# Kernel optimization log

Hardware: AMD Instinct MI355X
Metric: run time of the kernel (lower is better)

## Reference

```python
import jax, jax.numpy as jnp
import numpy as np

B, N, D, H = 2, 64, 256, 8
DK = D // H
EPS = 1e-5


def layer_norm(x, g, b):
    mu = jnp.mean(x, axis=-1, keepdims=True)
    var = jnp.var(x, axis=-1, keepdims=True)
    return (x - mu) * jax.lax.rsqrt(var + EPS) * g + b


def setup_inputs() -> dict:
    key = jax.random.key(0)
    ks = jax.random.split(key, 12)
    s = 1.0 / np.sqrt(D)
    inp = {
        "x": jax.random.normal(ks[0], (B, N, N, D), jnp.float32),
        "W_lk": jax.random.uniform(ks[1], (D, D), jnp.float32, -s, s),
        "W_rk": jax.random.uniform(ks[2], (D, D), jnp.float32, -s, s),
        "W_lv": jax.random.uniform(ks[3], (D, D), jnp.float32, -s, s),
        "W_rv": jax.random.uniform(ks[4], (D, D), jnp.float32, -s, s),
        "W_out": jax.random.uniform(ks[5], (D, D), jnp.float32, -s, s),
        "ln_agg_g": jnp.ones((D,), jnp.float32),
        "ln_agg_b": jnp.zeros((D,), jnp.float32),
        "W1": jax.random.uniform(ks[6], (D, 2 * D), jnp.float32, -s, s),
        "b1": jnp.zeros((2 * D,), jnp.float32),
        "W2": jax.random.uniform(ks[7], (2 * D, D), jnp.float32, -1.0 / np.sqrt(2 * D), 1.0 / np.sqrt(2 * D)),
        "b2": jnp.zeros((D,), jnp.float32),
        "ln2_g": jnp.ones((D,), jnp.float32),
        "ln2_b": jnp.zeros((D,), jnp.float32),
    }
    return inp


def reference(x, W_lk, W_rk, W_lv, W_rv, W_out, ln_agg_g, ln_agg_b, W1, b1, W2, b2, ln2_g, ln2_b):
    b, n = x.shape[0], x.shape[1]
    # projections (no bias), split into heads: [b, n, n, H, DK]
    lk = (x @ W_lk).reshape(b, n, n, H, DK)
    rk = (x @ W_rk).reshape(b, n, n, H, DK)
    lv = (x @ W_lv).reshape(b, n, n, H, DK)
    rv = (x @ W_rv).reshape(b, n, n, H, DK)
    # triangle attention scores over intermediate node 'a'
    scores = jnp.einsum('bxahd,bayhd->bxayh', lk, rk) / np.sqrt(DK)
    att = jax.nn.softmax(scores, axis=2)
    # fused triangle value aggregation: sum_a att * lv[x,a] * rv[a,y]
    o = jnp.einsum('bxayh,bxahd,bayhd->bxyhd', att, lv, rv)
    o = o.reshape(b, n, n, D) @ W_out
    # FFN block (dropout = 0)
    h = layer_norm(x + o, ln_agg_g, ln_agg_b)
    m = jax.nn.relu(h @ W1 + b1) @ W2 + b2
    return layer_norm(m + h, ln2_g, ln2_b)
```

## Files before the change

### kernel.cpp

```cpp
#include <hip/hip_runtime.h>

#define ROWS 8192
#define DIM  256

typedef short short8 __attribute__((ext_vector_type(8)));
typedef float f4     __attribute__((ext_vector_type(4)));

__device__ __forceinline__ float bf2f(unsigned int u16) {
    union { unsigned int i; float f; } v;
    v.i = (u16 & 0xffffu) << 16;
    return v.f;
}
__device__ __forceinline__ unsigned short f2bf(float f) {
    union { float f; unsigned int u; } v; v.f = f;
    unsigned int r = v.u + 0x7fffu + ((v.u >> 16) & 1u);
    return (unsigned short)(r >> 16);
}

__global__ __launch_bounds__(256)
void cast_all(const float* __restrict__ x, unsigned short* __restrict__ xb,
              const float* __restrict__ w0, const float* __restrict__ w1,
              const float* __restrict__ w2, const float* __restrict__ w3,
              const float* __restrict__ w4, const float* __restrict__ w5,
              const float* __restrict__ w6, unsigned short* __restrict__ wt)
{
    if (blockIdx.x < 2048) {
        const size_t i = ((size_t)blockIdx.x * 256 + threadIdx.x) * 4;
        float4 v = *(const float4*)(x + i);
        uint2 p;
        p.x = f2bf(v.x) | ((unsigned int)f2bf(v.y) << 16);
        p.y = f2bf(v.z) | ((unsigned int)f2bf(v.w) << 16);
        *(uint2*)(xb + i) = p;
        return;
    }
    __shared__ float t[32][33];
    int id = blockIdx.x - 2048;
    const float* src; int K, N, Ntiles; size_t doff;
    if (id < 320) {
        int w = id >> 6; id &= 63; K = 256; N = 256; Ntiles = 8;
        doff = (size_t)w * 65536;
        src = (w == 0) ? w0 : (w == 1) ? w1 : (w == 2) ? w2 : (w == 3) ? w3 : w4;
    } else if (id < 448) {
        id -= 320; K = 256; N = 512; Ntiles = 16; doff = 327680; src = w5;
    } else {
        id -= 448; K = 512; N = 256; Ntiles = 8;  doff = 458752; src = w6;
    }
    const int tk = id / Ntiles, tn = id % Ntiles;
    const int k0 = tk * 32, n0 = tn * 32;
    const int c = threadIdx.x & 31, r8 = threadIdx.x >> 5;
    for (int rr = r8; rr < 32; rr += 8)
        t[rr][c] = src[(size_t)(k0 + rr) * N + n0 + c];
    __syncthreads();
    for (int rr = r8; rr < 32; rr += 8)
        wt[doff + (size_t)(n0 + rr) * K + k0 + c] = f2bf(t[c][rr]);
}

__global__ __launch_bounds__(256)
void proj_mfma(const unsigned short* __restrict__ A, const unsigned short* __restrict__ WT,
               unsigned short* __restrict__ projT)
{
    const int lane = threadIdx.x & 63, wave = threadIdx.x >> 6;
    const int wsel = blockIdx.x >> 2;
    const int col0 = (blockIdx.x & 3) * 64;
    const int m0 = blockIdx.y * 128 + wave * 32;
    const int lm = lane & 15, lk8 = (lane >> 4) * 8;
    const unsigned short* W = WT + (size_t)wsel * 65536;
    unsigned short* dst = projT + (size_t)wsel * 2097152;

    f4 acc[2][4];
    #pragma unroll
    for (int i = 0; i < 2; ++i)
        #pragma unroll
        for (int j = 0; j < 4; ++j) acc[i][j] = (f4){0.f, 0.f, 0.f, 0.f};

    #pragma unroll 2
    for (int kc = 0; kc < 256; kc += 32) {
        short8 af[2], bf[4];
        #pragma unroll
        for (int i = 0; i < 2; ++i)
            af[i] = *(const short8*)(A + (size_t)(m0 + i * 16 + lm) * 256 + kc + lk8);
        #pragma unroll
        for (int j = 0; j < 4; ++j)
            bf[j] = *(const short8*)(W + (size_t)(col0 + j * 16 + lm) * 256 + kc + lk8);
        #pragma unroll
        for (int i = 0; i < 2; ++i)
            #pragma unroll
            for (int j = 0; j < 4; ++j)
                acc[i][j] = __builtin_amdgcn_mfma_f32_16x16x32_bf16(af[i], bf[j], acc[i][j], 0, 0, 0);
    }

    const int rbase = (lane >> 4) * 4;
    const int swap = (wsel == 3);
    #pragma unroll
    for (int i = 0; i < 2; ++i)
        #pragma unroll
        for (int j = 0; j < 4; ++j) {
            const int c = col0 + j * 16 + lm;
            const int h = c >> 5, d = c & 31;
            #pragma unroll
            for (int r = 0; r < 4; ++r) {
                const int m = m0 + i * 16 + rbase + r;
                const int b = m >> 12, ii = (m >> 6) & 63, jj = m & 63;
                const int p = swap ? jj : ii;
                const int q = swap ? ii : jj;
                const size_t idx = ((((size_t)b * 8 + h) * 64 + p) * 64 + q) * 32 + d;
                dst[idx] = f2bf(acc[i][j][r]);
            }
        }
}

__global__ __launch_bounds__(256)
void scores_mfma(const unsigned short* __restrict__ lkT, const unsigned short* __restrict__ rkT,
                 unsigned short* __restrict__ S)
{
    const int lane = threadIdx.x & 63, wave = threadIdx.x >> 6;
    const int bi = blockIdx.x;
    const int b = bi >> 7, h = (bi >> 4) & 7, a = (bi & 15) * 4 + wave;
    const size_t bh = (size_t)b * 8 + h;
    const int lm = lane & 15, lk8 = (lane >> 4) * 8;

    short8 af[4], bf[4];
    #pragma unroll
    for (int t = 0; t < 4; ++t) {
        af[t] = *(const short8*)(lkT + ((bh * 64 + (t * 16 + lm)) * 64 + a) * 32 + lk8);
        bf[t] = *(const short8*)(rkT + ((bh * 64 + a) * 64 + (t * 16 + lm)) * 32 + lk8);
    }
    const int rbase = (lane >> 4) * 4;
    unsigned short* Sb = S + bh * 262144 + a * 64;
    #pragma unroll
    for (int mt = 0; mt < 4; ++mt)
        #pragma unroll
        for (int nt = 0; nt < 4; ++nt) {
            f4 acc = (f4){0.f, 0.f, 0.f, 0.f};
            acc = __builtin_amdgcn_mfma_f32_16x16x32_bf16(af[mt], bf[nt], acc, 0, 0, 0);
            #pragma unroll
            for (int r = 0; r < 4; ++r) {
                const int xx = mt * 16 + rbase + r;
                const int yy = nt * 16 + lm;
                Sb[(size_t)xx * 4096 + yy] = f2bf(acc[r] * 0.17677669529663687f);
            }
        }
}

__global__ __launch_bounds__(256)
void softmax_agg(const unsigned short* __restrict__ S, const unsigned short* __restrict__ lvT,
                 const unsigned short* __restrict__ rvT, unsigned short* __restrict__ obuf)
{
    __shared__ float att[64][64];
    __shared__ float lvL[64][32];
    __shared__ float smx[4][64], ssm[4][64], invL[64];
    const int bi = blockIdx.x;
    const int b = bi >> 9, h = (bi >> 6) & 7, x = bi & 63;
    const size_t bh = (size_t)b * 8 + h;
    const int tid = threadIdx.x;

    {
        const int a = tid >> 2, yo = (tid & 3) * 16;
        const unsigned short* Sp = S + (bh * 64 + x) * 4096 + a * 64 + yo;
        uint4 p0 = *(const uint4*)(Sp);
        uint4 p1 = *(const uint4*)(Sp + 8);
        att[a][yo +  0] = bf2f(p0.x); att[a][yo +  1] = bf2f(p0.x >> 16);
        att[a][yo +  2] = bf2f(p0.y); att[a][yo +  3] = bf2f(p0.y >> 16);
        att[a][yo +  4] = bf2f(p0.z); att[a][yo +  5] = bf2f(p0.z >> 16);
        att[a][yo +  6] = bf2f(p0.w); att[a][yo +  7] = bf2f(p0.w >> 16);
        att[a][yo +  8] = bf2f(p1.x); att[a][yo +  9] = bf2f(p1.x >> 16);
        att[a][yo + 10] = bf2f(p1.y); att[a][yo + 11] = bf2f(p1.y >> 16);
        att[a][yo + 12] = bf2f(p1.z); att[a][yo + 13] = bf2f(p1.z >> 16);
        att[a][yo + 14] = bf2f(p1.w); att[a][yo + 15] = bf2f(p1.w >> 16);
        const int d0 = (tid & 3) * 8;
        uint4 q = *(const uint4*)(lvT + ((bh * 64 + x) * 64 + a) * 32 + d0);
        lvL[a][d0 + 0] = bf2f(q.x); lvL[a][d0 + 1] = bf2f(q.x >> 16);
        lvL[a][d0 + 2] = bf2f(q.y); lvL[a][d0 + 3] = bf2f(q.y >> 16);
        lvL[a][d0 + 4] = bf2f(q.z); lvL[a][d0 + 5] = bf2f(q.z >> 16);
        lvL[a][d0 + 6] = bf2f(q.w); lvL[a][d0 + 7] = bf2f(q.w >> 16);
    }
    __syncthreads();

    {
        const int y = tid & 63, az = tid >> 6;
        float mx = -1e30f;
        for (int a = az; a < 64; a += 4) mx = fmaxf(mx, att[a][y]);
        smx[az][y] = mx;
    }
    __syncthreads();

    {
        const int y = tid & 63, az = tid >> 6;
        const float mx = fmaxf(fmaxf(smx[0][y], smx[1][y]), fmaxf(smx[2][y], smx[3][y]));
        float s = 0.f;
        for (int a = az; a < 64; a += 4) {
            float e = __expf(att[a][y] - mx);
            att[a][y] = e;
            s += e;
        }
        ssm[az][y] = s;
    }
    __syncthreads();
    if (tid < 64)
        invL[tid] = 1.f / (ssm[0][tid] + ssm[1][tid] + ssm[2][tid] + ssm[3][tid]);
    __syncthreads();

    {
        const int dp = tid & 15, yb = tid >> 4;
        #pragma unroll
        for (int it = 0; it < 4; ++it) {
            const int y = yb + it * 16;
            const unsigned short* rvr = rvT + (bh * 64 + y) * 2048 + dp * 2;
            float a0 = 0.f, a1 = 0.f;
            #pragma unroll 8
            for (int a = 0; a < 64; ++a) {
                unsigned int pk = *(const unsigned int*)(rvr + a * 32);
                float w = att[a][y];
                a0 = fmaf(w * lvL[a][2 * dp],     bf2f(pk),       a0);
                a1 = fmaf(w * lvL[a][2 * dp + 1], bf2f(pk >> 16), a1);
            }
            const float inv = invL[y];
            a0 *= inv; a1 *= inv;
            unsigned int st = f2bf(a0) | ((unsigned int)f2bf(a1) << 16);
            *(unsigned int*)(obuf + (((size_t)b * 64 + x) * 64 + y) * 256 + h * 32 + dp * 2) = st;
        }
    }
}

__device__ __forceinline__ int swz8(int r, int c, int rl) {
    return r * rl + ((((c >> 3) ^ (r & 7)) << 3) | (c & 7));
}

__global__ __launch_bounds__(512, 2)
void ffn_fused(const unsigned short* __restrict__ A,
               const unsigned short* __restrict__ WoT,
               const unsigned short* __restrict__ W1T,
               const unsigned short* __restrict__ W2T,
               const float* __restrict__ xres,
               const float* __restrict__ g1, const float* __restrict__ be1,
               const float* __restrict__ b1, const float* __restrict__ b2,
               const float* __restrict__ g2, const float* __restrict__ be2,
               float* __restrict__ out)
{
    __shared__ unsigned short hs[32 * 256];
    __shared__ unsigned short ms[32 * 512];
    __shared__ float ps[32][8], pq[32][8];
    const int lane = threadIdx.x & 63, wave = threadIdx.x >> 6;
    const int m0 = blockIdx.x * 32;
    const int lm = lane & 15, lk8 = (lane >> 4) * 8;
    const int rbase = (lane >> 4) * 4;
    const int col0 = wave * 32;
    float hreg[2][2][4];

    {
        f4 acc[2][2];
        #pragma unroll
        for (int i = 0; i < 2; ++i)
            #pragma unroll
            for (int j = 0; j < 2; ++j) acc[i][j] = (f4){0.f, 0.f, 0.f, 0.f};
        #pragma unroll
        for (int kc = 0; kc < 256; kc += 32) {
            short8 af[2], bf[2];
            #pragma unroll
            for (int i = 0; i < 2; ++i)
                af[i] = *(const short8*)(A + (size_t)(m0 + i * 16 + lm) * 256 + kc + lk8);
            #pragma unroll
            for (int j = 0; j < 2; ++j)
                bf[j] = *(const short8*)(WoT + (size_t)(col0 + j * 16 + lm) * 256 + kc + lk8);
            #pragma unroll
            for (int i = 0; i < 2; ++i)
                #pragma unroll
                for (int j = 0; j < 2; ++j)
                    acc[i][j] = __builtin_amdgcn_mfma_f32_16x16x32_bf16(af[i], bf[j], acc[i][j], 0, 0, 0);
        }
        float v[2][2][4], s[2][4], q[2][4];
        #pragma unroll
        for (int i = 0; i < 2; ++i)
            #pragma unroll
            for (int r = 0; r < 4; ++r) { s[i][r] = 0.f; q[i][r] = 0.f; }
        #pragma unroll
        for (int i = 0; i < 2; ++i)
            #pragma unroll
            for (int j = 0; j < 2; ++j) {
                const int n = col0 + j * 16 + lm;
                #pragma unroll
                for (int r = 0; r < 4; ++r) {
                    const float t = acc[i][j][r] + xres[(size_t)(m0 + i * 16 + rbase + r) * 256 + n];
                    v[i][j][r] = t;
                    s[i][r] += t;
                    q[i][r] = fmaf(t, t, q[i][r]);
                }
            }
        #pragma unroll
        for (int off = 1; off < 16; off <<= 1)
            #pragma unroll
            for (int i = 0; i < 2; ++i)
                #pragma unroll
                for (int r = 0; r < 4; ++r) {
                    s[i][r] += __shfl_xor(s[i][r], off);
                    q[i][r] += __shfl_xor(q[i][r], off);
                }
        if (lm == 0)
            #pragma unroll
            for (int i = 0; i < 2; ++i)
                #pragma unroll
                for (int r = 0; r < 4; ++r) {
                    ps[i * 16 + rbase + r][wave] = s[i][r];
                    pq[i * 16 + rbase + r][wave] = q[i][r];
                }
        __syncthreads();
        #pragma unroll
        for (int i = 0; i < 2; ++i)
            #pragma unroll
            for (int r = 0; r < 4; ++r) {
                const int lr = i * 16 + rbase + r;
                const float Sm = ps[lr][0] + ps[lr][1] + ps[lr][2] + ps[lr][3]
                               + ps[lr][4] + ps[lr][5] + ps[lr][6] + ps[lr][7];
                const float Qm = pq[lr][0] + pq[lr][1] + pq[lr][2] + pq[lr][3]
                               + pq[lr][4] + pq[lr][5] + pq[lr][6] + pq[lr][7];
                const float mu = Sm * (1.f / 256.f);
                const float ri = rsqrtf(Qm * (1.f / 256.f) - mu * mu + 1e-5f);
                #pragma unroll
                for (int j = 0; j < 2; ++j) {
                    const int n = col0 + j * 16 + lm;
                    const unsigned short hb16 = f2bf((v[i][j][r] - mu) * ri * g1[n] + be1[n]);
                    hs[swz8(lr, n, 256)] = hb16;
                    hreg[i][j][r] = bf2f(hb16);
                }
            }
    }
    __syncthreads();

    {
        const int c0 = wave * 64;
        f4 acc2[2][4];
        #pragma unroll
        for (int i = 0; i < 2; ++i)
            #pragma unroll
            for (int j = 0; j < 4; ++j) acc2[i][j] = (f4){0.f, 0.f, 0.f, 0.f};
        #pragma unroll
        for (int kc = 0; kc < 256; kc += 32) {
            short8 af[2], bf[4];
            #pragma unroll
            for (int i = 0; i < 2; ++i)
                af[i] = *(const short8*)(hs + swz8(i * 16 + lm, kc + lk8, 256));
            #pragma unroll
            for (int j = 0; j < 4; ++j)
                bf[j] = *(const short8*)(W1T + (size_t)(c0 + j * 16 + lm) * 256 + kc + lk8);
            #pragma unroll
            for (int i = 0; i < 2; ++i)
                #pragma unroll
                for (int j = 0; j < 4; ++j)
                    acc2[i][j] = __builtin_amdgcn_mfma_f32_16x16x32_bf16(af[i], bf[j], acc2[i][j], 0, 0, 0);
        }
        #pragma unroll
        for (int i = 0; i < 2; ++i)
            #pragma unroll
            for (int j = 0; j < 4; ++j) {
                const int n = c0 + j * 16 + lm;
                const float bb = b1[n];
                #pragma unroll
                for (int r = 0; r < 4; ++r)
                    ms[swz8(i * 16 + rbase + r, n, 512)] = f2bf(fmaxf(acc2[i][j][r] + bb, 0.f));
            }
    }
    __syncthreads();

    {
        f4 acc[2][2];
        #pragma unroll
        for (int i = 0; i < 2; ++i)
            #pragma unroll
            for (int j = 0; j < 2; ++j) acc[i][j] = (f4){0.f, 0.f, 0.f, 0.f};
        #pragma unroll
        for (int kc = 0; kc < 512; kc += 32) {
            short8 af[2], bf[2];
            #pragma unroll
            for (int i = 0; i < 2; ++i)
                af[i] = *(const short8*)(ms + swz8(i * 16 + lm, kc + lk8, 512));
            #pragma unroll
            for (int j = 0; j < 2; ++j)
                bf[j] = *(const short8*)(W2T + (size_t)(col0 + j * 16 + lm) * 512 + kc + lk8);
            #pragma unroll
            for (int i = 0; i < 2; ++i)
                #pragma unroll
                for (int j = 0; j < 2; ++j)
                    acc[i][j] = __builtin_amdgcn_mfma_f32_16x16x32_bf16(af[i], bf[j], acc[i][j], 0, 0, 0);
        }
        float v[2][2][4], s[2][4], q[2][4];
        #pragma unroll
        for (int i = 0; i < 2; ++i)
            #pragma unroll
            for (int r = 0; r < 4; ++r) { s[i][r] = 0.f; q[i][r] = 0.f; }
        #pragma unroll
        for (int i = 0; i < 2; ++i)
            #pragma unroll
            for (int j = 0; j < 2; ++j) {
                const int n = col0 + j * 16 + lm;
                const float bb = b2[n];
                #pragma unroll
                for (int r = 0; r < 4; ++r) {
                    const float t = acc[i][j][r] + bb + hreg[i][j][r];
                    v[i][j][r] = t;
                    s[i][r] += t;
                    q[i][r] = fmaf(t, t, q[i][r]);
                }
            }
        #pragma unroll
        for (int off = 1; off < 16; off <<= 1)
            #pragma unroll
            for (int i = 0; i < 2; ++i)
                #pragma unroll
                for (int r = 0; r < 4; ++r) {
                    s[i][r] += __shfl_xor(s[i][r], off);
                    q[i][r] += __shfl_xor(q[i][r], off);
                }
        if (lm == 0)
            #pragma unroll
            for (int i = 0; i < 2; ++i)
                #pragma unroll
                for (int r = 0; r < 4; ++r) {
                    ps[i * 16 + rbase + r][wave] = s[i][r];
                    pq[i * 16 + rbase + r][wave] = q[i][r];
                }
        __syncthreads();
        #pragma unroll
        for (int i = 0; i < 2; ++i)
            #pragma unroll
            for (int r = 0; r < 4; ++r) {
                const int lr = i * 16 + rbase + r;
                const float Sm = ps[lr][0] + ps[lr][1] + ps[lr][2] + ps[lr][3]
                               + ps[lr][4] + ps[lr][5] + ps[lr][6] + ps[lr][7];
                const float Qm = pq[lr][0] + pq[lr][1] + pq[lr][2] + pq[lr][3]
                               + pq[lr][4] + pq[lr][5] + pq[lr][6] + pq[lr][7];
                const float mu = Sm * (1.f / 256.f);
                const float ri = rsqrtf(Qm * (1.f / 256.f) - mu * mu + 1e-5f);
                const int m = m0 + lr;
                #pragma unroll
                for (int j = 0; j < 2; ++j) {
                    const int n = col0 + j * 16 + lm;
                    out[(size_t)m * 256 + n] = (v[i][j][r] - mu) * ri * g2[n] + be2[n];
                }
            }
    }
}

extern "C" void kernel_launch(void* const* d_in, const int* in_sizes, int n_in,
                              void* d_out, int out_size, void* d_ws, size_t ws_size,
                              hipStream_t stream)
{
    const float* x    = (const float*)d_in[0];
    const float* Wlk  = (const float*)d_in[1];
    const float* Wrk  = (const float*)d_in[2];
    const float* Wlv  = (const float*)d_in[3];
    const float* Wrv  = (const float*)d_in[4];
    const float* Wout = (const float*)d_in[5];
    const float* g1   = (const float*)d_in[6];
    const float* be1  = (const float*)d_in[7];
    const float* W1   = (const float*)d_in[8];
    const float* b1   = (const float*)d_in[9];
    const float* W2   = (const float*)d_in[10];
    const float* b2   = (const float*)d_in[11];
    const float* g2   = (const float*)d_in[12];
    const float* be2  = (const float*)d_in[13];

    char* base = (char*)d_ws;
    const size_t MB = 1ull << 20;
    unsigned short* xb    = (unsigned short*)(base + 0);
    unsigned short* obufb = (unsigned short*)(base + 0);
    unsigned short* projT = (unsigned short*)(base + 4 * MB);
    unsigned short* lkT   = projT;
    unsigned short* rkT   = projT + 2097152;
    unsigned short* lvT   = projT + 2 * 2097152;
    unsigned short* rvT   = projT + 3 * 2097152;
    unsigned short* Sbuf  = (unsigned short*)(base + 32 * MB);
    unsigned short* WT    = (unsigned short*)(base + 40 * MB);

    cast_all<<<2624, 256, 0, stream>>>(x, xb, Wlk, Wrk, Wlv, Wrv, Wout, W1, W2, WT);
    proj_mfma<<<dim3(16, 64), 256, 0, stream>>>(xb, WT, projT);
    scores_mfma<<<256, 256, 0, stream>>>(lkT, rkT, Sbuf);
    softmax_agg<<<1024, 256, 0, stream>>>(Sbuf, lvT, rvT, obufb);
    ffn_fused<<<256, 512, 0, stream>>>(obufb, WT + 262144, WT + 327680, WT + 458752,
                                       x, g1, be1, b1, b2, g2, be2, (float*)d_out);
}
```

Baseline: 167.2 us.

## Process four x rows per softmax_agg block to reuse rv loads

Each softmax_agg block now handles four x rows at once with 512 threads. Every rv element is loaded once from global memory and used for four accumulators, which cuts rv traffic fourfold. The cost is more LDS per block (about 100KB), fewer blocks (256), and more registers, so occupancy may drop.

```diff
diff --git a/kernel.cpp b/kernel.cpp
--- a/kernel.cpp
+++ b/kernel.cpp
@@ -142,82 +142,99 @@
         }
 }
 
-__global__ __launch_bounds__(256)
+__global__ __launch_bounds__(512)
 void softmax_agg(const unsigned short* __restrict__ S, const unsigned short* __restrict__ lvT,
                  const unsigned short* __restrict__ rvT, unsigned short* __restrict__ obuf)
 {
-    __shared__ float att[64][64];
-    __shared__ float lvL[64][32];
-    __shared__ float smx[4][64], ssm[4][64], invL[64];
+    __shared__ float att[4][64][64];
+    __shared__ float lvL[4][64][32];
+    __shared__ float smx[4][2][64], ssm[4][2][64], invL[4][64];
     const int bi = blockIdx.x;
-    const int b = bi >> 9, h = (bi >> 6) & 7, x = bi & 63;
+    const int b = bi >> 7, h = (bi >> 4) & 7, xq = bi & 15;
+    const int x0 = xq * 4;
     const size_t bh = (size_t)b * 8 + h;
     const int tid = threadIdx.x;
 
     {
-        const int a = tid >> 2, yo = (tid & 3) * 16;
-        const unsigned short* Sp = S + (bh * 64 + x) * 4096 + a * 64 + yo;
-        uint4 p0 = *(const uint4*)(Sp);
-        uint4 p1 = *(const uint4*)(Sp + 8);
-        att[a][yo +  0] = bf2f(p0.x); att[a][yo +  1] = bf2f(p0.x >> 16);
-        att[a][yo +  2] = bf2f(p0.y); att[a][yo +  3] = bf2f(p0.y >> 16);
-        att[a][yo +  4] = bf2f(p0.z); att[a][yo +  5] = bf2f(p0.z >> 16);
-        att[a][yo +  6] = bf2f(p0.w); att[a][yo +  7] = bf2f(p0.w >> 16);
-        att[a][yo +  8] = bf2f(p1.x); att[a][yo +  9] = bf2f(p1.x >> 16);
-        att[a][yo + 10] = bf2f(p1.y); att[a][yo + 11] = bf2f(p1.y >> 16);
-        att[a][yo + 12] = bf2f(p1.z); att[a][yo + 13] = bf2f(p1.z >> 16);
-        att[a][yo + 14] = bf2f(p1.w); att[a][yo + 15] = bf2f(p1.w >> 16);
-        const int d0 = (tid & 3) * 8;
-        uint4 q = *(const uint4*)(lvT + ((bh * 64 + x) * 64 + a) * 32 + d0);
-        lvL[a][d0 + 0] = bf2f(q.x); lvL[a][d0 + 1] = bf2f(q.x >> 16);
-        lvL[a][d0 + 2] = bf2f(q.y); lvL[a][d0 + 3] = bf2f(q.y >> 16);
-        lvL[a][d0 + 4] = bf2f(q.z); lvL[a][d0 + 5] = bf2f(q.z >> 16);
-        lvL[a][d0 + 6] = bf2f(q.w); lvL[a][d0 + 7] = bf2f(q.w >> 16);
-    }
-    __syncthreads();
-
-    {
-        const int y = tid & 63, az = tid >> 6;
+        const int xi = tid >> 7;
+        const int t2 = tid & 127;
+        const int a = t2 >> 1;
+        const int yo = (t2 & 1) * 32;
+        const unsigned short* Sp = S + (bh * 64 + (x0 + xi)) * 4096 + a * 64 + yo;
+        #pragma unroll
+        for (int u = 0; u < 4; ++u) {
+            uint4 p = *(const uint4*)(Sp + u * 8);
+            float* d = &att[xi][a][yo + u * 8];
+            d[0] = bf2f(p.x); d[1] = bf2f(p.x >> 16);
+            d[2] = bf2f(p.y); d[3] = bf2f(p.y >> 16);
+            d[4] = bf2f(p.z); d[5] = bf2f(p.z >> 16);
+            d[6] = bf2f(p.w); d[7] = bf2f(p.w >> 16);
+        }
+        const int d0 = (t2 & 1) * 16;
+        const unsigned short* Lp = lvT + ((bh * 64 + (x0 + xi)) * 64 + a) * 32 + d0;
+        #pragma unroll
+        for (int u = 0; u < 2; ++u) {
+            uint4 q = *(const uint4*)(Lp + u * 8);
+            float* d = &lvL[xi][a][d0 + u * 8];
+            d[0] = bf2f(q.x); d[1] = bf2f(q.x >> 16);
+            d[2] = bf2f(q.y); d[3] = bf2f(q.y >> 16);
+            d[4] = bf2f(q.z); d[5] = bf2f(q.z >> 16);
+            d[6] = bf2f(q.w); d[7] = bf2f(q.w >> 16);
+        }
+    }
+    __syncthreads();
+
+    {
+        const int xi = tid >> 7, az = (tid >> 6) & 1, y = tid & 63;
         float mx = -1e30f;
-        for (int a = az; a < 64; a += 4) mx = fmaxf(mx, att[a][y]);
-        smx[az][y] = mx;
-    }
-    __syncthreads();
-
-    {
-        const int y = tid & 63, az = tid >> 6;
-        const float mx = fmaxf(fmaxf(smx[0][y], smx[1][y]), fmaxf(smx[2][y], smx[3][y]));
+        for (int a = az; a < 64; a += 2) mx = fmaxf(mx, att[xi][a][y]);
+        smx[xi][az][y] = mx;
+    }
+    __syncthreads();
+
+    {
+        const int xi = tid >> 7, az = (tid >> 6) & 1, y = tid & 63;
+        const float mx = fmaxf(smx[xi][0][y], smx[xi][1][y]);
         float s = 0.f;
-        for (int a = az; a < 64; a += 4) {
-            float e = __expf(att[a][y] - mx);
-            att[a][y] = e;
+        for (int a = az; a < 64; a += 2) {
+            float e = __expf(att[xi][a][y] - mx);
+            att[xi][a][y] = e;
             s += e;
         }
-        ssm[az][y] = s;
-    }
-    __syncthreads();
-    if (tid < 64)
-        invL[tid] = 1.f / (ssm[0][tid] + ssm[1][tid] + ssm[2][tid] + ssm[3][tid]);
+        ssm[xi][az][y] = s;
+    }
+    __syncthreads();
+    if (tid < 256) {
+        const int xi = tid >> 6, y = tid & 63;
+        invL[xi][y] = 1.f / (ssm[xi][0][y] + ssm[xi][1][y]);
+    }
     __syncthreads();
 
     {
         const int dp = tid & 15, yb = tid >> 4;
         #pragma unroll
-        for (int it = 0; it < 4; ++it) {
-            const int y = yb + it * 16;
+        for (int it = 0; it < 2; ++it) {
+            const int y = yb + it * 32;
             const unsigned short* rvr = rvT + (bh * 64 + y) * 2048 + dp * 2;
-            float a0 = 0.f, a1 = 0.f;
-            #pragma unroll 8
+            float a0[4] = {0.f, 0.f, 0.f, 0.f}, a1[4] = {0.f, 0.f, 0.f, 0.f};
+            #pragma unroll 4
             for (int a = 0; a < 64; ++a) {
                 unsigned int pk = *(const unsigned int*)(rvr + a * 32);
-                float w = att[a][y];
-                a0 = fmaf(w * lvL[a][2 * dp],     bf2f(pk),       a0);
-                a1 = fmaf(w * lvL[a][2 * dp + 1], bf2f(pk >> 16), a1);
-            }
-            const float inv = invL[y];
-            a0 *= inv; a1 *= inv;
-            unsigned int st = f2bf(a0) | ((unsigned int)f2bf(a1) << 16);
-            *(unsigned int*)(obuf + (((size_t)b * 64 + x) * 64 + y) * 256 + h * 32 + dp * 2) = st;
+                const float lo = bf2f(pk), hi = bf2f(pk >> 16);
+                #pragma unroll
+                for (int xi = 0; xi < 4; ++xi) {
+                    const float w = att[xi][a][y];
+                    const float2 lv2 = *(const float2*)&lvL[xi][a][2 * dp];
+                    a0[xi] = fmaf(w * lv2.x, lo, a0[xi]);
+                    a1[xi] = fmaf(w * lv2.y, hi, a1[xi]);
+                }
+            }
+            #pragma unroll
+            for (int xi = 0; xi < 4; ++xi) {
+                const float inv = invL[xi][y];
+                unsigned int st = f2bf(a0[xi] * inv) | ((unsigned int)f2bf(a1[xi] * inv) << 16);
+                *(unsigned int*)(obuf + (((size_t)b * 64 + (x0 + xi)) * 64 + y) * 256 + h * 32 + dp * 2) = st;
+            }
         }
     }
 }
@@ -474,7 +491,7 @@
     cast_all<<<2624, 256, 0, stream>>>(x, xb, Wlk, Wrk, Wlv, Wrv, Wout, W1, W2, WT);
     proj_mfma<<<dim3(16, 64), 256, 0, stream>>>(xb, WT, projT);
     scores_mfma<<<256, 256, 0, stream>>>(lkT, rkT, Sbuf);
-    softmax_agg<<<1024, 256, 0, stream>>>(Sbuf, lvT, rvT, obufb);
+    softmax_agg<<<256, 512, 0, stream>>>(Sbuf, lvT, rvT, obufb);
     ffn_fused<<<256, 512, 0, stream>>>(obufb, WT + 262144, WT + 327680, WT + 458752,
                                        x, g1, be1, b1, b2, g2, be2, (float*)d_out);
 }
```

After: 170.8 us. 2.1% more time.
